# Kernel tuning notes

Hardware: AMD Instinct MI355X
Metric: run time of the kernel (lower is better)

## Reference

```python
import jax, jax.numpy as jnp
import numpy as np

N_NODES = 10000
N_EDGES = 160000
FEAT = 32
EMB = 32
VOCAB = 32000
EDGE_DIM = 9
HID = 32  # edge MLP hidden


def setup_inputs() -> dict:
    key = jax.random.key(0)
    ks = jax.random.split(key, 16)
    s = lambda *sh: 1.0 / np.sqrt(sh[0])
    inp = {
        "signal": jax.random.randint(ks[0], (1,), 0, VOCAB, dtype=jnp.int64) if jax.config.jax_enable_x64 else jax.random.randint(ks[0], (1,), 0, VOCAB).astype(jnp.int32),
        "x": jax.random.normal(ks[1], (N_NODES, FEAT), dtype=jnp.float32),
        "edge_index": jax.random.randint(ks[2], (2, N_EDGES), 0, N_NODES).astype(jnp.int32),
        "edge_attr": jax.random.normal(ks[3], (N_EDGES, EDGE_DIM), dtype=jnp.float32),
        # edge MLP 1: 9 -> 32 -> FEAT*EMB
        "w1a": jax.random.normal(ks[4], (EDGE_DIM, HID), dtype=jnp.float32) * s(EDGE_DIM),
        "b1a": jnp.zeros((HID,), jnp.float32),
        "w1b": jax.random.normal(ks[5], (HID, FEAT * EMB), dtype=jnp.float32) * s(HID),
        "b1b": jnp.zeros((FEAT * EMB,), jnp.float32),
        "root1": jax.random.normal(ks[6], (FEAT, EMB), dtype=jnp.float32) * s(FEAT),
        "bias1": jnp.zeros((EMB,), jnp.float32),
        # edge MLP 2: 9 -> 32 -> EMB*EMB
        "w2a": jax.random.normal(ks[7], (EDGE_DIM, HID), dtype=jnp.float32) * s(EDGE_DIM),
        "b2a": jnp.zeros((HID,), jnp.float32),
        "w2b": jax.random.normal(ks[8], (HID, EMB * EMB), dtype=jnp.float32) * s(HID),
        "b2b": jnp.zeros((EMB * EMB,), jnp.float32),
        "root2": jax.random.normal(ks[9], (EMB, EMB), dtype=jnp.float32) * s(EMB),
        "bias2": jnp.zeros((EMB,), jnp.float32),
        "emb_table": jax.random.normal(ks[10], (VOCAB, EMB), dtype=jnp.float32),
    }
    return inp


def nnconv(x, edge_index, edge_attr, wa, ba, wb, bb, root, bias, in_ch, out_ch):
    # edge MLP -> per-edge weight matrices [E, in_ch, out_ch]
    h = jax.nn.relu(edge_attr @ wa + ba)
    W_e = (h @ wb + bb).reshape(-1, in_ch, out_ch)
    src, dst = edge_index[0], edge_index[1]
    # gather source node features, per-edge matmul
    msg = jnp.einsum("ei,eio->eo", x[src], W_e)  # [E, out_ch]
    summed = jax.ops.segment_sum(msg, dst, num_segments=N_NODES)
    cnt = jax.ops.segment_sum(jnp.ones((msg.shape[0],), msg.dtype), dst, num_segments=N_NODES)
    aggr = summed / jnp.maximum(cnt, 1.0)[:, None]  # scatter-mean (0 for isolated nodes)
    return aggr + x @ root + bias


def reference(signal, x, edge_index, edge_attr,
              w1a, b1a, w1b, b1b, root1, bias1,
              w2a, b2a, w2b, b2b, root2, bias2, emb_table):
    h = jax.nn.relu(nnconv(x, edge_index, edge_attr, w1a, b1a, w1b, b1b, root1, bias1, FEAT, EMB))
    h = jax.nn.relu(nnconv(h, edge_index, edge_attr, w2a, b2a, w2b, b2b, root2, bias2, EMB, EMB))
    sig = emb_table[signal]          # [1, EMB]
    sig = sig[0]                      # squeeze leading 1 (matches torch branch)
    scores = h @ sig                  # [N]
    return jax.nn.log_softmax(scores, axis=0)
```

## Files before the change

### kernel.cpp

```cpp
#include <hip/hip_runtime.h>
#include <math.h>

#define NN 10000
#define NE 160000
#define C  32
#define ED 9
#define EAP 12

typedef __attribute__((ext_vector_type(8))) short short8v;
typedef __attribute__((ext_vector_type(4))) float float4v;

__device__ inline unsigned short f2bf(float f) {
    unsigned int u = __float_as_uint(f);
    return (unsigned short)((u + 0x7fffu + ((u >> 16) & 1u)) >> 16);
}
__device__ inline float bf2f(unsigned int us) { return __uint_as_float(us << 16); }

__global__ __launch_bounds__(1024) void setup_kernel(const int* __restrict__ ei,
                                                     int* __restrict__ offs,
                                                     int* __restrict__ doffs,
                                                     const float* __restrict__ w1b,
                                                     const float* __restrict__ w2b,
                                                     unsigned short* __restrict__ wbB1,
                                                     unsigned short* __restrict__ wbB2,
                                                     uint4* __restrict__ zcur) {
    __shared__ int cnt[NN];
    __shared__ int wtot[16];
    const int b = blockIdx.x, t = threadIdx.x;
    if (b < 2) {
        for (int i = t; i < NN; i += 1024) cnt[i] = 0;
        __syncthreads();
        const int* col = ei + (b ? NE : 0);
        for (int e = t; e < NE; e += 1024) atomicAdd(&cnt[col[e]], 1);
        __syncthreads();
        int* out = b ? doffs : offs;
        const int lane = t & 63, wid = t >> 6;
        const int base = t * 10;
        int loc[10];
        int s = 0;
#pragma unroll
        for (int j = 0; j < 10; ++j) {
            int v = (base + j < NN) ? cnt[base + j] : 0;
            loc[j] = s;
            s += v;
        }
        int inc = s;
        for (int d = 1; d < 64; d <<= 1) {
            int v = __shfl_up(inc, d, 64);
            if (lane >= d) inc += v;
        }
        if (lane == 63) wtot[wid] = inc;
        __syncthreads();
        if (t < 16) {
            int w = wtot[t];
            for (int d = 1; d < 16; d <<= 1) {
                int v = __shfl_up(w, d, 64);
                if (t >= d) w += v;
            }
            wtot[t] = w;
        }
        __syncthreads();
        const int excl = inc - s + (wid ? wtot[wid - 1] : 0);
#pragma unroll
        for (int j = 0; j < 10; ++j)
            if (base + j < NN) out[base + j] = excl + loc[j];
        if (t == 1023) out[NN] = wtot[15];
    } else if (b < 34) {
        const int idx = (b - 2) * 1024 + t;
        const int i = idx & 31, j = idx >> 5;
        wbB1[idx] = f2bf(w1b[(j & 31) * (C * C) + i * C + (j >> 5)]);
    } else if (b < 66) {
        const int idx = (b - 34) * 1024 + t;
        const int i = idx & 31, j = idx >> 5;
        wbB2[idx] = f2bf(w2b[(j & 31) * (C * C) + i * C + (j >> 5)]);
    } else {
        const int i = (b - 66) * 1024 + t;
        if (i < 5016) zcur[i] = uint4{0u, 0u, 0u, 0u};
    }
}

__device__ __forceinline__ void u_mfma_core(int nb, int tid,
                                            const float* __restrict__ xs,
                                            unsigned int* __restrict__ bhi,
                                            unsigned int* __restrict__ blo,
                                            const unsigned short* __restrict__ wbB,
                                            const float* __restrict__ bb,
                                            unsigned short* __restrict__ UT,
                                            float* __restrict__ xb) {
    {
        const float vx = xs[2 * tid], vy = xs[2 * tid + 1];
        const unsigned hx = f2bf(vx), hy = f2bf(vy);
        bhi[tid] = hx | (hy << 16);
        const float lx = vx - bf2f(hx), ly = vy - bf2f(hy);
        blo[tid] = (unsigned)f2bf(lx) | ((unsigned)f2bf(ly) << 16);
    }
    __syncthreads();

    const int w = tid >> 6, l = tid & 63;
    const int r15 = l & 15, q = l >> 4;
    const short8v Bh = *reinterpret_cast<const short8v*>(
        reinterpret_cast<const unsigned short*>(bhi) + r15 * C + q * 8);
    const short8v Bl = *reinterpret_cast<const short8v*>(
        reinterpret_cast<const unsigned short*>(blo) + r15 * C + q * 8);
    const float4v Z = {0.f, 0.f, 0.f, 0.f};

#pragma unroll
    for (int cg = 0; cg < 4; ++cg) {
        const int jbase = w * 256 + cg * 64;
#pragma unroll
        for (int t4 = 0; t4 < 4; ++t4) {
            const int jb = jbase + t4 * 16;
            const short8v A = *reinterpret_cast<const short8v*>(
                wbB + (size_t)(jb + r15) * C + q * 8);
            float4v acc = __builtin_amdgcn_mfma_f32_16x16x32_bf16(A, Bl, Z, 0, 0, 0);
            acc = __builtin_amdgcn_mfma_f32_16x16x32_bf16(A, Bh, acc, 0, 0, 0);
            ushort4 pk;
            pk.x = f2bf(acc[0]); pk.y = f2bf(acc[1]);
            pk.z = f2bf(acc[2]); pk.w = f2bf(acc[3]);
            *reinterpret_cast<ushort4*>(UT + (size_t)(nb + r15) * (C * C) + jb + q * 4) = pk;
        }
    }
#pragma unroll
    for (int t = 0; t < 2; ++t) {
        const int idx = t * 256 + tid;
        const int n = idx >> 5, oo = idx & 31;
        float acc = 0.f;
#pragma unroll
        for (int i = 0; i < C; ++i) acc += xs[n * C + i] * bb[i * C + oo];
        xb[(size_t)(nb + n) * C + oo] = acc;
    }
}

__global__ __launch_bounds__(256) void mid_kernel(const int* __restrict__ ei,
                                                  const float* __restrict__ ea,
                                                  const int* __restrict__ offs,
                                                  const int* __restrict__ doffs,
                                                  int* __restrict__ cur_src,
                                                  int* __restrict__ cur_dst,
                                                  int* __restrict__ pd,
                                                  float* __restrict__ ea_s,
                                                  const float* __restrict__ xin,
                                                  const unsigned short* __restrict__ wbB,
                                                  const float* __restrict__ bb,
                                                  unsigned short* __restrict__ UT,
                                                  float* __restrict__ xb) {
    __shared__ float xs[16 * C];
    __shared__ unsigned int bhi[256], blo[256];
    const int b = blockIdx.x, tid = threadIdx.x;
    if (b < 625) {
        const int e = b * 256 + tid;
        if (e < NE) {
            const int sn  = ei[e];
            const int dn  = ei[NE + e];
            const int pos = offs[sn]  + atomicAdd(&cur_src[sn], 1);
            const int dpo = doffs[dn] + atomicAdd(&cur_dst[dn], 1);
            pd[pos] = dpo;
#pragma unroll
            for (int j = 0; j < ED; ++j)
                ea_s[(size_t)pos * EAP + j] = ea[(size_t)e * ED + j];
        }
    } else {
        const int nb = (b - 625) * 16;
        const float2 v = *reinterpret_cast<const float2*>(xin + nb * C + 2 * tid);
        xs[2 * tid] = v.x; xs[2 * tid + 1] = v.y;
        __syncthreads();
        u_mfma_core(nb, tid, xs, bhi, blo, wbB, bb, UT, xb);
    }
}

__global__ __launch_bounds__(256) void edge5_kernel(const int* __restrict__ offs,
                                                    const int* __restrict__ pd,
                                                    const float* __restrict__ ea_s,
                                                    const float* __restrict__ wa,
                                                    const float* __restrict__ ba,
                                                    const unsigned short* __restrict__ UT,
                                                    const float* __restrict__ xb,
                                                    float* __restrict__ msg) {
    __shared__ float was[ED * C];
    __shared__ float bas[C];
    const int tid = threadIdx.x;
    for (int t = tid; t < ED * C; t += 256) was[t] = wa[t];
    if (tid < C) bas[tid] = ba[tid];
    __syncthreads();

    const int w  = tid >> 6;
    const int l  = tid & 63;
    const int s  = blockIdx.x * 4 + w;
    const int q  = l >> 4;
    const int el = l & 15;

    const int e0 = offs[s], e1 = offs[s + 1];
    if (e0 == e1) return;

    const unsigned short* up = UT + (size_t)s * (C * C);
    const short8v B1 = *reinterpret_cast<const short8v*>(up + el * C + q * 8);
    const short8v B2 = *reinterpret_cast<const short8v*>(up + (el + 16) * C + q * 8);
    const float c1 = xb[s * C + el];
    const float c2 = xb[s * C + el + 16];
    const float4v C1 = {c1, c1, c1, c1};
    const float4v C2 = {c2, c2, c2, c2};
    float hb[8];
#pragma unroll
    for (int i = 0; i < 8; ++i) hb[i] = bas[q * 8 + i];

    for (int pb = e0; pb < e1; pb += 16) {
        const int p  = pb + el;
        const int pc = (p < e1) ? p : e0;
        const float* eap = ea_s + (size_t)pc * EAP;
        const float4v ea0 = *reinterpret_cast<const float4v*>(eap);
        const float4v ea1 = *reinterpret_cast<const float4v*>(eap + 4);
        const float   ea8 = eap[8];

        float h[8];
#pragma unroll
        for (int i = 0; i < 8; ++i) h[i] = hb[i];
#pragma unroll
        for (int j = 0; j < ED; ++j) {
            const float ev = (j == 0) ? ea0.x : (j == 1) ? ea0.y : (j == 2) ? ea0.z
                           : (j == 3) ? ea0.w : (j == 4) ? ea1.x : (j == 5) ? ea1.y
                           : (j == 6) ? ea1.z : (j == 7) ? ea1.w : ea8;
            const float4v w0 = *reinterpret_cast<const float4v*>(&was[j * C + q * 8]);
            const float4v w1 = *reinterpret_cast<const float4v*>(&was[j * C + q * 8 + 4]);
            h[0] += ev * w0.x; h[1] += ev * w0.y; h[2] += ev * w0.z; h[3] += ev * w0.w;
            h[4] += ev * w1.x; h[5] += ev * w1.y; h[6] += ev * w1.z; h[7] += ev * w1.w;
        }
        union { int u[4]; short8v v; } A;
#pragma unroll
        for (int v = 0; v < 4; ++v) {
            const unsigned lo = f2bf(fmaxf(h[2 * v], 0.f));
            const unsigned hi = f2bf(fmaxf(h[2 * v + 1], 0.f));
            A.u[v] = (int)(lo | (hi << 16));
        }
        const float4v d1 = __builtin_amdgcn_mfma_f32_16x16x32_bf16(A.v, B1, C1, 0, 0, 0);
        const float4v d2 = __builtin_amdgcn_mfma_f32_16x16x32_bf16(A.v, B2, C2, 0, 0, 0);
#pragma unroll
        for (int r = 0; r < 4; ++r) {
            const int pe = pb + q * 4 + r;
            if (pe < e1) {
                const int mr = pd[pe];
                msg[(size_t)mr * C + el]      = d1[r];
                msg[(size_t)mr * C + el + 16] = d2[r];
            }
        }
    }
}

__global__ __launch_bounds__(256) void naggu_kernel(const int* __restrict__ doffs,
                                                    const float* __restrict__ msg,
                                                    const float* __restrict__ xin,
                                                    const float* __restrict__ root1,
                                                    const float* __restrict__ bias1,
                                                    const unsigned short* __restrict__ wbB2,
                                                    const float* __restrict__ b2b,
                                                    unsigned short* __restrict__ UT,
                                                    float* __restrict__ xb,
                                                    float* __restrict__ h1out) {
    __shared__ float rs[C * C];
    __shared__ float bs[C];
    __shared__ float xs[16 * C];
    __shared__ float xls[4][C];
    __shared__ unsigned int bhi[256], blo[256];
    const int tid = threadIdx.x;
    for (int t = tid; t < C * C; t += 256) rs[t] = root1[t];
    if (tid < C) bs[tid] = bias1[tid];
    __syncthreads();

    const int w = tid >> 6, lane = tid & 63;
    const int half = lane >> 5, o = lane & 31;
    const int nb = blockIdx.x * 16;

    for (int r = 0; r < 4; ++r) {
        const int d = nb + w * 4 + r;
        const int e0 = doffs[d], e1 = doffs[d + 1];
        float acc = 0.f;
        for (int p = e0 + half; p < e1; p += 2) acc += msg[(size_t)p * C + o];
        acc += __shfl_down(acc, 32, 64);
        if (lane < 32) xls[w][o] = xin[(size_t)d * C + o];
        if (lane < 32) {
            const float cn = fmaxf((float)(e1 - e0), 1.f);
            float a = bs[o] + acc / cn;
#pragma unroll
            for (int i = 0; i < C; ++i) a += xls[w][i] * rs[i * C + o];
            const float hv = fmaxf(a, 0.f);
            xs[(w * 4 + r) * C + o] = hv;
            h1out[(size_t)d * C + o] = hv;
        }
    }
    __syncthreads();

    u_mfma_core(nb, tid, xs, bhi, blo, wbB2, b2b, UT, xb);
}

__global__ __launch_bounds__(256) void nodeagg2_score(const int* __restrict__ doffs,
                                                      const float* __restrict__ msg,
                                                      const float* __restrict__ h1,
                                                      const float* __restrict__ root,
                                                      const float* __restrict__ bias,
                                                      const float* __restrict__ emb,
                                                      const int* __restrict__ signal,
                                                      float* __restrict__ scores) {
    __shared__ float rs[C * C];
    __shared__ float bs[C];
    __shared__ float sig[C];
    __shared__ float xls[4][C];
    const int tid = threadIdx.x;
    for (int t = tid; t < C * C; t += 256) rs[t] = root[t];
    if (tid < C) {
        bs[tid]  = bias[tid];
        sig[tid] = emb[(size_t)signal[0] * C + tid];
    }
    __syncthreads();

    const int w = tid >> 6, lane = tid & 63;
    const int half = lane >> 5, o = lane & 31;
    const int d = blockIdx.x * 4 + w;
    const int e0 = doffs[d], e1 = doffs[d + 1];

    float acc = 0.f;
    for (int p = e0 + half; p < e1; p += 2) acc += msg[(size_t)p * C + o];
    acc += __shfl_down(acc, 32, 64);
    if (lane < 32) xls[w][o] = h1[(size_t)d * C + o];
    if (lane < 32) {
        const float cn = fmaxf((float)(e1 - e0), 1.f);
        float a = bs[o] + acc / cn;
#pragma unroll
        for (int i = 0; i < C; ++i) a += xls[w][i] * rs[i * C + o];
        float val = fmaxf(a, 0.f) * sig[o];
#pragma unroll
        for (int off = 16; off; off >>= 1) val += __shfl_xor(val, off, 32);
        if (o == 0) scores[d] = val;
    }
}

__global__ __launch_bounds__(1024) void reduce_out_kernel(const float* __restrict__ scores,
                                                          float* __restrict__ out) {
    __shared__ float sm[16];
    __shared__ float ss[16];
    const int tid = threadIdx.x;
    float m = -INFINITY;
    for (int n = tid; n < NN; n += 1024) m = fmaxf(m, scores[n]);
    for (int off = 32; off; off >>= 1) m = fmaxf(m, __shfl_down(m, off, 64));
    if ((tid & 63) == 0) sm[tid >> 6] = m;
    __syncthreads();
    if (tid == 0) {
        float mm = sm[0];
        for (int w = 1; w < 16; ++w) mm = fmaxf(mm, sm[w]);
        sm[0] = mm;
    }
    __syncthreads();
    const float gmax = sm[0];
    float s = 0.f;
    for (int n = tid; n < NN; n += 1024) s += expf(scores[n] - gmax);
    for (int off = 32; off; off >>= 1) s += __shfl_down(s, off, 64);
    if ((tid & 63) == 0) ss[tid >> 6] = s;
    __syncthreads();
    if (tid == 0) {
        float t = 0.f;
        for (int w = 0; w < 16; ++w) t += ss[w];
        ss[0] = logf(t);
    }
    __syncthreads();
    const float sub = gmax + ss[0];
    for (int n = tid; n < NN; n += 1024) out[n] = scores[n] - sub;
}

extern "C" void kernel_launch(void* const* d_in, const int* in_sizes, int n_in,
                              void* d_out, int out_size, void* d_ws, size_t ws_size,
                              hipStream_t stream) {
    const int*   signal = (const int*)d_in[0];
    const float* x      = (const float*)d_in[1];
    const int*   ei     = (const int*)d_in[2];
    const float* ea     = (const float*)d_in[3];
    const float* w1a    = (const float*)d_in[4];
    const float* b1a    = (const float*)d_in[5];
    const float* w1b    = (const float*)d_in[6];
    const float* b1b    = (const float*)d_in[7];
    const float* root1  = (const float*)d_in[8];
    const float* bias1  = (const float*)d_in[9];
    const float* w2a    = (const float*)d_in[10];
    const float* b2a    = (const float*)d_in[11];
    const float* w2b    = (const float*)d_in[12];
    const float* b2b    = (const float*)d_in[13];
    const float* root2  = (const float*)d_in[14];
    const float* bias2  = (const float*)d_in[15];
    const float* emb    = (const float*)d_in[16];

    float* ws = (float*)d_ws;
    unsigned short* UT = (unsigned short*)ws;
    float* msg     = ws + 5120000;
    float* xb      = ws + 10240000;
    float* h1      = ws + 10560000;
    float* ea_s    = ws + 10880000;
    unsigned short* wbB1 = (unsigned short*)(ws + 12800000);
    unsigned short* wbB2 = (unsigned short*)(ws + 12816384);
    float* scores  = ws + 12832768;
    int*   offs    = (int*)(ws + 12842768);
    int*   doffs   = (int*)(ws + 12852784);
    int*   pd      = (int*)(ws + 12862800);
    int*   cur_src = (int*)(ws + 13022800);
    int*   cur_dst = cur_src + NN;

    setup_kernel<<<71, 1024, 0, stream>>>(ei, offs, doffs, w1b, w2b, wbB1, wbB2,
                                          (uint4*)cur_src);
    mid_kernel<<<1250, 256, 0, stream>>>(ei, ea, offs, doffs, cur_src, cur_dst,
                                         pd, ea_s, x, wbB1, b1b, UT, xb);
    edge5_kernel<<<2500, 256, 0, stream>>>(offs, pd, ea_s, w1a, b1a, UT, xb, msg);
    naggu_kernel<<<625, 256, 0, stream>>>(doffs, msg, x, root1, bias1,
                                          wbB2, b2b, UT, xb, h1);
    edge5_kernel<<<2500, 256, 0, stream>>>(offs, pd, ea_s, w2a, b2a, UT, xb, msg);
    nodeagg2_score<<<2500, 256, 0, stream>>>(doffs, msg, h1, root2, bias2,
                                             emb, signal, scores);
    reduce_out_kernel<<<1, 1024, 0, stream>>>(scores, (float*)d_out);
}
```

Baseline: 161.0 us.

## Split setup into parallel histogram, scan and prep kernels

The degree histogram used to be built by only two 1024-thread blocks, each looping over all 160k edges with shared-memory atomics. It is now a grid-wide kernel using global atomics, followed by a separate two-block scan kernel and a prep kernel that zeroes the counters and cursors and converts the weights to bf16. This spreads the serial histogram work across the whole GPU. In exchange it adds two kernel launches and contended global atomics.

After: 144.8 us. -10.0%, faster.

```diff
diff --git a/kernel.cpp b/kernel.cpp
--- a/kernel.cpp
+++ b/kernel.cpp
@@ -16,67 +16,76 @@
 }
 __device__ inline float bf2f(unsigned int us) { return __uint_as_float(us << 16); }
 
-__global__ __launch_bounds__(1024) void setup_kernel(const int* __restrict__ ei,
-                                                     int* __restrict__ offs,
-                                                     int* __restrict__ doffs,
-                                                     const float* __restrict__ w1b,
-                                                     const float* __restrict__ w2b,
-                                                     unsigned short* __restrict__ wbB1,
-                                                     unsigned short* __restrict__ wbB2,
-                                                     uint4* __restrict__ zcur) {
-    __shared__ int cnt[NN];
-    __shared__ int wtot[16];
-    const int b = blockIdx.x, t = threadIdx.x;
-    if (b < 2) {
-        for (int i = t; i < NN; i += 1024) cnt[i] = 0;
-        __syncthreads();
-        const int* col = ei + (b ? NE : 0);
-        for (int e = t; e < NE; e += 1024) atomicAdd(&cnt[col[e]], 1);
-        __syncthreads();
-        int* out = b ? doffs : offs;
-        const int lane = t & 63, wid = t >> 6;
-        const int base = t * 10;
-        int loc[10];
-        int s = 0;
-#pragma unroll
-        for (int j = 0; j < 10; ++j) {
-            int v = (base + j < NN) ? cnt[base + j] : 0;
-            loc[j] = s;
-            s += v;
-        }
-        int inc = s;
-        for (int d = 1; d < 64; d <<= 1) {
-            int v = __shfl_up(inc, d, 64);
-            if (lane >= d) inc += v;
-        }
-        if (lane == 63) wtot[wid] = inc;
-        __syncthreads();
-        if (t < 16) {
-            int w = wtot[t];
-            for (int d = 1; d < 16; d <<= 1) {
-                int v = __shfl_up(w, d, 64);
-                if (t >= d) w += v;
-            }
-            wtot[t] = w;
-        }
-        __syncthreads();
-        const int excl = inc - s + (wid ? wtot[wid - 1] : 0);
-#pragma unroll
-        for (int j = 0; j < 10; ++j)
-            if (base + j < NN) out[base + j] = excl + loc[j];
-        if (t == 1023) out[NN] = wtot[15];
-    } else if (b < 34) {
-        const int idx = (b - 2) * 1024 + t;
+#define ZQ 10016
+__global__ __launch_bounds__(256) void prep_kernel(uint4* __restrict__ zreg,
+                                                   const float* __restrict__ w1b,
+                                                   const float* __restrict__ w2b,
+                                                   unsigned short* __restrict__ wbB1,
+                                                   unsigned short* __restrict__ wbB2) {
+    const int b = blockIdx.x, tid = threadIdx.x;
+    if (b < 40) {
+        const int i = b * 256 + tid;
+        if (i < ZQ) zreg[i] = uint4{0u, 0u, 0u, 0u};
+    } else if (b < 168) {
+        const int idx = (b - 40) * 256 + tid;
         const int i = idx & 31, j = idx >> 5;
         wbB1[idx] = f2bf(w1b[(j & 31) * (C * C) + i * C + (j >> 5)]);
-    } else if (b < 66) {
-        const int idx = (b - 34) * 1024 + t;
+    } else {
+        const int idx = (b - 168) * 256 + tid;
         const int i = idx & 31, j = idx >> 5;
         wbB2[idx] = f2bf(w2b[(j & 31) * (C * C) + i * C + (j >> 5)]);
-    } else {
-        const int i = (b - 66) * 1024 + t;
-        if (i < 5016) zcur[i] = uint4{0u, 0u, 0u, 0u};
-    }
+    }
+}
+
+__global__ __launch_bounds__(256) void hist_kernel(const int* __restrict__ ei,
+                                                   int* __restrict__ cnt_src,
+                                                   int* __restrict__ cnt_dst) {
+    const int e = blockIdx.x * 256 + threadIdx.x;
+    if (e < NE) {
+        atomicAdd(&cnt_src[ei[e]], 1);
+        atomicAdd(&cnt_dst[ei[NE + e]], 1);
+    }
+}
+
+__global__ __launch_bounds__(1024) void scan2_kernel(const int* __restrict__ cnt_src,
+                                                     const int* __restrict__ cnt_dst,
+                                                     int* __restrict__ offs,
+                                                     int* __restrict__ doffs) {
+    const int* cnt = blockIdx.x ? cnt_dst : cnt_src;
+    int* out       = blockIdx.x ? doffs   : offs;
+    __shared__ int wtot[16];
+    const int t = threadIdx.x;
+    const int lane = t & 63, wid = t >> 6;
+    const int base = t * 10;
+    int loc[10];
+    int s = 0;
+#pragma unroll
+    for (int j = 0; j < 10; ++j) {
+        int v = (base + j < NN) ? cnt[base + j] : 0;
+        loc[j] = s;
+        s += v;
+    }
+    int inc = s;
+    for (int d = 1; d < 64; d <<= 1) {
+        int v = __shfl_up(inc, d, 64);
+        if (lane >= d) inc += v;
+    }
+    if (lane == 63) wtot[wid] = inc;
+    __syncthreads();
+    if (t < 16) {
+        int w = wtot[t];
+        for (int d = 1; d < 16; d <<= 1) {
+            int v = __shfl_up(w, d, 64);
+            if (t >= d) w += v;
+        }
+        wtot[t] = w;
+    }
+    __syncthreads();
+    const int excl = inc - s + (wid ? wtot[wid - 1] : 0);
+#pragma unroll
+    for (int j = 0; j < 10; ++j)
+        if (base + j < NN) out[base + j] = excl + loc[j];
+    if (t == 1023) out[NN] = wtot[15];
 }
 
 __device__ __forceinline__ void u_mfma_core(int nb, int tid,
@@ -397,11 +406,14 @@
     int*   offs    = (int*)(ws + 12842768);
     int*   doffs   = (int*)(ws + 12852784);
     int*   pd      = (int*)(ws + 12862800);
-    int*   cur_src = (int*)(ws + 13022800);
+    int*   cnt_src = (int*)(ws + 13022800);
+    int*   cnt_dst = cnt_src + NN;
+    int*   cur_src = cnt_dst + NN;
     int*   cur_dst = cur_src + NN;
 
-    setup_kernel<<<71, 1024, 0, stream>>>(ei, offs, doffs, w1b, w2b, wbB1, wbB2,
-                                          (uint4*)cur_src);
+    prep_kernel<<<296, 256, 0, stream>>>((uint4*)cnt_src, w1b, w2b, wbB1, wbB2);
+    hist_kernel<<<(NE + 255) / 256, 256, 0, stream>>>(ei, cnt_src, cnt_dst);
+    scan2_kernel<<<2, 1024, 0, stream>>>(cnt_src, cnt_dst, offs, doffs);
     mid_kernel<<<1250, 256, 0, stream>>>(ei, ea, offs, doffs, cur_src, cur_dst,
                                          pd, ea_s, x, wbB1, b1b, UT, xb);
     edge5_kernel<<<2500, 256, 0, stream>>>(offs, pd, ea_s, w1a, b1a, UT, xb, msg);
```
